# Kernel optimization log

Hardware: AMD Instinct MI355X
Metric: run time of the kernel (lower is better)

The kernel has to match this reference:

```python
import jax, jax.numpy as jnp
import numpy as np

D_MODEL = 2048
N_HEADS = 16
HEAD_DIM = D_MODEL // N_HEADS
SCALE = HEAD_DIM ** -0.5


def setup_inputs() -> dict:
    key = jax.random.key(0)
    ks = jax.random.split(key, 9)
    B, L, D = 4, 4096, D_MODEL
    s = 1.0 / np.sqrt(D)
    inp = {"x": jax.random.normal(ks[0], (B, L, D), dtype=jnp.float32)}
    inp["Wq"] = jax.random.normal(ks[1], (D, D), dtype=jnp.float32) * s
    inp["bq"] = jnp.zeros((D,), dtype=jnp.float32)
    inp["Wk"] = jax.random.normal(ks[2], (D, D), dtype=jnp.float32) * s
    inp["bk"] = jnp.zeros((D,), dtype=jnp.float32)
    inp["Wv"] = jax.random.normal(ks[3], (D, D), dtype=jnp.float32) * s
    inp["bv"] = jnp.zeros((D,), dtype=jnp.float32)
    inp["Wo"] = jax.random.normal(ks[4], (D, D), dtype=jnp.float32) * s
    inp["bo"] = jnp.zeros((D,), dtype=jnp.float32)
    return inp


def reference(x, Wq, bq, Wk, bk, Wv, bv, Wo, bo):
    B, L, D = x.shape
    H, Hd = N_HEADS, HEAD_DIM
    # projections (torch Linear: x @ W.T + b)
    q = jnp.einsum('bld,ed->ble', x, Wq) + bq
    k = jnp.einsum('bld,ed->ble', x, Wk) + bk
    v = jnp.einsum('bld,ed->ble', x, Wv) + bv
    phi_q = jax.nn.elu(q) + 1.0
    phi_k = jax.nn.elu(k) + 1.0
    # (B, L, H, Hd)
    phi_q = phi_q.reshape(B, L, H, Hd)
    phi_k = phi_k.reshape(B, L, H, Hd)
    v = v.reshape(B, L, H, Hd)
    # elementwise prefix sum over sequence dim
    kv_sum = jnp.cumsum(phi_k * v, axis=1)  # (B, L, H, Hd)
    context = (phi_q * kv_sum).reshape(B, L, D) * SCALE
    return jnp.einsum('bld,ed->ble', context, Wo) + bo
```

## Files before the change

kernel.cpp:

```cpp
#include <hip/hip_runtime.h>
#include <hip/hip_bf16.h>
#include <cstdint>
#include <cstddef>

typedef __bf16 bf16x8 __attribute__((ext_vector_type(8)));
typedef __bf16 bf16x4 __attribute__((ext_vector_type(4)));
typedef float  f32x4  __attribute__((ext_vector_type(4)));

#define D_MODEL 2048
#define SEQ     4096
#define BATCH   4
#define M_TOK   (BATCH * SEQ)
#define ATTN_SCALE 0.08838834764831845f

#define BM 128
#define BN 128
#define BK 64

#define NSEG   64
#define SEGLEN (SEQ / NSEG)

__device__ __forceinline__ void async_load16(const void* g, void* l) {
    __builtin_amdgcn_global_load_lds(
        (const __attribute__((address_space(1))) unsigned int*)g,
        (__attribute__((address_space(3))) unsigned int*)l,
        16, 0, 0);
}

__global__ __launch_bounds__(256) void k_cast_bf16(const float* __restrict__ in,
                                                   __bf16* __restrict__ out,
                                                   int n8) {
    int i = blockIdx.x * 256 + threadIdx.x;
    if (i >= n8) return;
    const float4* in4 = (const float4*)in;
    float4 a = in4[2 * i];
    float4 b = in4[2 * i + 1];
    bf16x8 o;
    o[0] = (__bf16)a.x; o[1] = (__bf16)a.y; o[2] = (__bf16)a.z; o[3] = (__bf16)a.w;
    o[4] = (__bf16)b.x; o[5] = (__bf16)b.y; o[6] = (__bf16)b.z; o[7] = (__bf16)b.w;
    ((bf16x8*)out)[i] = o;
}

__global__ __launch_bounds__(256) void k_cast_w4(const float* __restrict__ w0,
                                                 const float* __restrict__ w1,
                                                 const float* __restrict__ w2,
                                                 const float* __restrict__ w3,
                                                 __bf16* __restrict__ out, int n8) {
    const float* srcs[4] = {w0, w1, w2, w3};
    const float* in = srcs[blockIdx.y];
    __bf16* o = out + (size_t)blockIdx.y * (size_t)n8 * 8;
    int i = blockIdx.x * 256 + threadIdx.x;
    if (i >= n8) return;
    const float4* in4 = (const float4*)in;
    float4 a = in4[2 * i];
    float4 b = in4[2 * i + 1];
    bf16x8 v;
    v[0] = (__bf16)a.x; v[1] = (__bf16)a.y; v[2] = (__bf16)a.z; v[3] = (__bf16)a.w;
    v[4] = (__bf16)b.x; v[5] = (__bf16)b.y; v[6] = (__bf16)b.z; v[7] = (__bf16)b.w;
    ((bf16x8*)o)[i] = v;
}

template <int PHI, typename OUT_T>
__device__ __forceinline__ void gemm_bt(const __bf16* __restrict__ A,
                                        const __bf16* __restrict__ Bm,
                                        const float* __restrict__ bias,
                                        OUT_T* __restrict__ C,
                                        int K, int N) {
    __shared__ __align__(16) __bf16 As[BM * BK];
    __shared__ __align__(16) __bf16 Bs[BN * BK];

    const int tid  = threadIdx.x;
    const int lane = tid & 63;
    const int wave = tid >> 6;
    const int waveM = wave & 1;
    const int waveN = wave >> 1;
    const long bm = (long)blockIdx.y * BM;
    const long bn = (long)blockIdx.x * BN;

    const int srow  = tid >> 3;
    const int sphys = tid & 7;
    const __bf16* gA[4]; const __bf16* gB[4];
    __bf16* lA[4]; __bf16* lB[4];
#pragma unroll
    for (int q = 0; q < 4; q++) {
        int r  = q * 32 + srow;
        int cb = (sphys ^ (r & 7)) * 8;
        gA[q] = A  + (bm + r) * (long)K + cb;
        gB[q] = Bm + (bn + r) * (long)K + cb;
        lA[q] = As + q * 2048 + tid * 8;
        lB[q] = Bs + q * 2048 + tid * 8;
    }

    const int mrow = waveM * 64 + (lane & 15);
    const int nrow = waveN * 64 + (lane & 15);
    const int ksel = lane >> 4;

    f32x4 acc[4][4] = {};

    for (int k0 = 0; k0 < K; k0 += BK) {
#pragma unroll
        for (int q = 0; q < 4; q++) async_load16(gA[q] + k0, lA[q]);
#pragma unroll
        for (int q = 0; q < 4; q++) async_load16(gB[q] + k0, lB[q]);
        __syncthreads();

#pragma unroll
        for (int s = 0; s < 2; s++) {
            bf16x8 af[4], bfr[4];
#pragma unroll
            for (int i = 0; i < 4; i++) {
                int r = mrow + i * 16;
                int p = (s * 4 + ksel) ^ (r & 7);
                af[i] = *(const bf16x8*)(As + r * 64 + p * 8);
            }
#pragma unroll
            for (int j = 0; j < 4; j++) {
                int r = nrow + j * 16;
                int p = (s * 4 + ksel) ^ (r & 7);
                bfr[j] = *(const bf16x8*)(Bs + r * 64 + p * 8);
            }
#pragma unroll
            for (int i = 0; i < 4; i++)
#pragma unroll
                for (int j = 0; j < 4; j++)
                    acc[i][j] = __builtin_amdgcn_mfma_f32_16x16x32_bf16(
                        af[i], bfr[j], acc[i][j], 0, 0, 0);
        }
        __syncthreads();
    }

    const int r0 = (lane >> 4) * 4;
    const int cn = lane & 15;
#pragma unroll
    for (int i = 0; i < 4; i++) {
        long mg = bm + waveM * 64 + i * 16 + r0;
#pragma unroll
        for (int j = 0; j < 4; j++) {
            long ng = bn + waveN * 64 + j * 16 + cn;
            float bia = bias[ng];
#pragma unroll
            for (int r = 0; r < 4; r++) {
                float v = acc[i][j][r] + bia;
                if (PHI) v = (v > 0.f) ? (v + 1.f) : __expf(v);
                C[(mg + r) * (long)N + ng] = (OUT_T)v;
            }
        }
    }
}

__global__ __launch_bounds__(256) void k_gemm_qkv(
    const __bf16* __restrict__ xb,
    const __bf16* __restrict__ wq, const __bf16* __restrict__ wk, const __bf16* __restrict__ wv,
    const float* __restrict__ bq, const float* __restrict__ bk, const float* __restrict__ bv,
    __bf16* __restrict__ oq, __bf16* __restrict__ ok, __bf16* __restrict__ ov) {
    const int z = blockIdx.z;
    const __bf16* W = (z == 0) ? wq : (z == 1) ? wk : wv;
    const float*  b = (z == 0) ? bq : (z == 1) ? bk : bv;
    __bf16*       o = (z == 0) ? oq : (z == 1) ? ok : ov;
    if (z < 2)
        gemm_bt<1, __bf16>(xb, W, b, o, D_MODEL, D_MODEL);
    else
        gemm_bt<0, __bf16>(xb, W, b, o, D_MODEL, D_MODEL);
}

__global__ __launch_bounds__(256) void k_gemm_out(
    const __bf16* __restrict__ ctx, const __bf16* __restrict__ wo,
    const float* __restrict__ bo, float* __restrict__ out) {
    gemm_bt<0, float>(ctx, wo, bo, out, D_MODEL, D_MODEL);
}

__global__ __launch_bounds__(256) void k_scan_partial(
    const __bf16* __restrict__ phik, const __bf16* __restrict__ v,
    float* __restrict__ partial) {
    const int b  = blockIdx.z;
    const int s  = blockIdx.y;
    const int c0 = blockIdx.x * 1024 + threadIdx.x * 4;
    long base = ((long)b * SEQ + (long)s * SEGLEN) * D_MODEL + c0;
    const bf16x4* pk = (const bf16x4*)(phik + base);
    const bf16x4* pv = (const bf16x4*)(v + base);
    float s0 = 0, s1 = 0, s2 = 0, s3 = 0;
    for (int l = 0; l < SEGLEN; l++) {
        bf16x4 a = *pk, w = *pv;
        s0 += (float)a[0] * (float)w[0];
        s1 += (float)a[1] * (float)w[1];
        s2 += (float)a[2] * (float)w[2];
        s3 += (float)a[3] * (float)w[3];
        pk += D_MODEL / 4; pv += D_MODEL / 4;
    }
    *(float4*)(partial + ((long)(b * NSEG + s)) * D_MODEL + c0) = make_float4(s0, s1, s2, s3);
}

__global__ __launch_bounds__(256) void k_scan_apply(
    const __bf16* __restrict__ phiq,
    __bf16* phik_ctx,
    const __bf16* __restrict__ v,
    const float* __restrict__ partial) {
    const int b  = blockIdx.z;
    const int s  = blockIdx.y;
    const int c0 = blockIdx.x * 1024 + threadIdx.x * 4;
    float r0 = 0, r1 = 0, r2 = 0, r3 = 0;
    for (int sp = 0; sp < s; sp++) {
        float4 p = *(const float4*)(partial + ((long)(b * NSEG + sp)) * D_MODEL + c0);
        r0 += p.x; r1 += p.y; r2 += p.z; r3 += p.w;
    }
    long base = ((long)b * SEQ + (long)s * SEGLEN) * D_MODEL + c0;
    bf16x4* pk = (bf16x4*)(phik_ctx + base);
    const bf16x4* pv = (const bf16x4*)(v + base);
    const bf16x4* pq = (const bf16x4*)(phiq + base);
    for (int l = 0; l < SEGLEN; l++) {
        bf16x4 a = *pk, w = *pv, q = *pq;
        r0 += (float)a[0] * (float)w[0];
        r1 += (float)a[1] * (float)w[1];
        r2 += (float)a[2] * (float)w[2];
        r3 += (float)a[3] * (float)w[3];
        bf16x4 o;
        o[0] = (__bf16)((float)q[0] * r0 * ATTN_SCALE);
        o[1] = (__bf16)((float)q[1] * r1 * ATTN_SCALE);
        o[2] = (__bf16)((float)q[2] * r2 * ATTN_SCALE);
        o[3] = (__bf16)((float)q[3] * r3 * ATTN_SCALE);
        *pk = o;
        pk += D_MODEL / 4; pv += D_MODEL / 4; pq += D_MODEL / 4;
    }
}

extern "C" void kernel_launch(void* const* d_in, const int* in_sizes, int n_in,
                              void* d_out, int out_size, void* d_ws, size_t ws_size,
                              hipStream_t stream) {
    const float* x  = (const float*)d_in[0];
    const float* Wq = (const float*)d_in[1];
    const float* bq = (const float*)d_in[2];
    const float* Wk = (const float*)d_in[3];
    const float* bk = (const float*)d_in[4];
    const float* Wv = (const float*)d_in[5];
    const float* bv = (const float*)d_in[6];
    const float* Wo = (const float*)d_in[7];
    const float* bo = (const float*)d_in[8];

    const size_t XB = (size_t)M_TOK * D_MODEL;
    const size_t WB = (size_t)D_MODEL * D_MODEL;

    char* p = (char*)d_ws;
    __bf16* xb   = (__bf16*)p; p += XB * 2;
    __bf16* wqb  = (__bf16*)p; p += WB * 2;
    __bf16* wkb  = (__bf16*)p; p += WB * 2;
    __bf16* wvb  = (__bf16*)p; p += WB * 2;
    __bf16* wob  = (__bf16*)p; p += WB * 2;
    __bf16* phiq = (__bf16*)p; p += XB * 2;
    __bf16* phik = (__bf16*)p; p += XB * 2;
    __bf16* vb   = (__bf16*)p; p += XB * 2;
    if ((size_t)(p - (char*)d_ws) > ws_size) return;

    float*  partial = (float*)xb;
    __bf16* ctx     = phik;

    k_cast_bf16<<<dim3((unsigned)(XB / 8 / 256)), 256, 0, stream>>>(x, xb, (int)(XB / 8));
    k_cast_w4<<<dim3((unsigned)(WB / 8 / 256), 4), 256, 0, stream>>>(Wq, Wk, Wv, Wo, wqb, (int)(WB / 8));

    k_gemm_qkv<<<dim3(D_MODEL / BN, M_TOK / BM, 3), 256, 0, stream>>>(
        xb, wqb, wkb, wvb, bq, bk, bv, phiq, phik, vb);

    k_scan_partial<<<dim3(2, NSEG, BATCH), 256, 0, stream>>>(phik, vb, partial);
    k_scan_apply<<<dim3(2, NSEG, BATCH), 256, 0, stream>>>(phiq, phik, vb, partial);

    k_gemm_out<<<dim3(D_MODEL / BN, M_TOK / BM, 1), 256, 0, stream>>>(
        ctx, wob, bo, (float*)d_out);
}
```

Measured before the change: 928.9 us.

## Fuse QKV projections into one 768-thread block sharing the A tile

The QKV GEMM now runs one 768-thread block per output tile, with three wave groups computing Q, K and V from a single shared A tile. This removes the triple loading of x from global memory into LDS. BK is halved to 32 with a new XOR swizzle, and launch bounds request 4 blocks per CU to raise occupancy. The scan segment count is doubled for more parallelism. In exchange, each k-step carries less work per barrier, and the larger block may limit residency.

After: 1.099 ms. 18.4% more time.

```diff
diff --git a/kernel.cpp b/kernel.cpp
--- a/kernel.cpp
+++ b/kernel.cpp
@@ -15,9 +15,9 @@
 
 #define BM 128
 #define BN 128
-#define BK 64
-
-#define NSEG   64
+#define BK 32
+
+#define NSEG   128
 #define SEGLEN (SEQ / NSEG)
 
 __device__ __forceinline__ void async_load16(const void* g, void* l) {
@@ -26,6 +26,7 @@
         (__attribute__((address_space(3))) unsigned int*)l,
         16, 0, 0);
 }
+__device__ __forceinline__ int swz(int r) { return (r >> 1) & 3; }
 
 __global__ __launch_bounds__(256) void k_cast_bf16(const float* __restrict__ in,
                                                    __bf16* __restrict__ out,
@@ -60,12 +61,99 @@
     ((bf16x8*)o)[i] = v;
 }
 
-template <int PHI, typename OUT_T>
-__device__ __forceinline__ void gemm_bt(const __bf16* __restrict__ A,
-                                        const __bf16* __restrict__ Bm,
-                                        const float* __restrict__ bias,
-                                        OUT_T* __restrict__ C,
-                                        int K, int N) {
+__global__ __launch_bounds__(768, 4) void k_gemm_qkv(
+    const __bf16* __restrict__ A,
+    const __bf16* __restrict__ wq, const __bf16* __restrict__ wk, const __bf16* __restrict__ wv,
+    const float* __restrict__ bq, const float* __restrict__ bk, const float* __restrict__ bv,
+    __bf16* __restrict__ oq, __bf16* __restrict__ ok, __bf16* __restrict__ ov) {
+    __shared__ __align__(16) __bf16 As[BM * BK];
+    __shared__ __align__(16) __bf16 Bs[3 * BN * BK];
+
+    const int tid  = threadIdx.x;
+    const int lane = tid & 63;
+    const int wave = tid >> 6;
+    const int zw   = wave >> 2;
+    const int quad = wave & 3;
+    const int waveM = quad & 1;
+    const int waveN = quad >> 1;
+    const long bm = (long)blockIdx.y * BM;
+    const long bn = (long)blockIdx.x * BN;
+    const int K = D_MODEL, N = D_MODEL;
+
+    const int ar = tid >> 2, apc = tid & 3;
+    const __bf16* gA = A + (bm + ar) * (long)K + (long)((apc ^ swz(ar)) * 8);
+    __bf16* lA = As + tid * 8;
+    const __bf16* gB[2]; __bf16* lB[2];
+#pragma unroll
+    for (int u = 0; u < 2; u++) {
+        int cb = tid + u * 768;
+        int z  = cb >> 9;
+        int w  = cb & 511;
+        int r  = w >> 2, pc = w & 3;
+        const __bf16* Wz = (z == 0) ? wq : (z == 1) ? wk : wv;
+        gB[u] = Wz + (bn + r) * (long)K + (long)((pc ^ swz(r)) * 8);
+        lB[u] = Bs + cb * 8;
+    }
+
+    const int ksel = lane >> 4;
+    int offA[4], offB[4];
+#pragma unroll
+    for (int i = 0; i < 4; i++) {
+        int r = waveM * 64 + (lane & 15) + 16 * i;
+        offA[i] = r * BK + (ksel ^ swz(r)) * 8;
+    }
+#pragma unroll
+    for (int j = 0; j < 4; j++) {
+        int r = waveN * 64 + (lane & 15) + 16 * j;
+        offB[j] = zw * (BN * BK) + r * BK + (ksel ^ swz(r)) * 8;
+    }
+
+    f32x4 acc[4][4] = {};
+
+    for (int k0 = 0; k0 < K; k0 += BK) {
+        if (tid < 512) async_load16(gA + k0, lA);
+        async_load16(gB[0] + k0, lB[0]);
+        async_load16(gB[1] + k0, lB[1]);
+        __syncthreads();
+
+        bf16x8 af[4], bfr[4];
+#pragma unroll
+        for (int i = 0; i < 4; i++) af[i]  = *(const bf16x8*)(As + offA[i]);
+#pragma unroll
+        for (int j = 0; j < 4; j++) bfr[j] = *(const bf16x8*)(Bs + offB[j]);
+#pragma unroll
+        for (int i = 0; i < 4; i++)
+#pragma unroll
+            for (int j = 0; j < 4; j++)
+                acc[i][j] = __builtin_amdgcn_mfma_f32_16x16x32_bf16(
+                    af[i], bfr[j], acc[i][j], 0, 0, 0);
+        __syncthreads();
+    }
+
+    const float* bias = (zw == 0) ? bq : (zw == 1) ? bk : bv;
+    __bf16*      Co   = (zw == 0) ? oq : (zw == 1) ? ok : ov;
+    const int r0 = (lane >> 4) * 4;
+    const int cn = lane & 15;
+#pragma unroll
+    for (int i = 0; i < 4; i++) {
+        long mg = bm + waveM * 64 + i * 16 + r0;
+#pragma unroll
+        for (int j = 0; j < 4; j++) {
+            long ng = bn + waveN * 64 + j * 16 + cn;
+            float bia = bias[ng];
+#pragma unroll
+            for (int r = 0; r < 4; r++) {
+                float v = acc[i][j][r] + bia;
+                if (zw < 2) v = (v > 0.f) ? (v + 1.f) : __expf(v);
+                Co[(mg + r) * (long)N + ng] = (__bf16)v;
+            }
+        }
+    }
+}
+
+__global__ __launch_bounds__(256, 4) void k_gemm_out(
+    const __bf16* __restrict__ A, const __bf16* __restrict__ Bm,
+    const float* __restrict__ bias, float* __restrict__ C) {
     __shared__ __align__(16) __bf16 As[BM * BK];
     __shared__ __align__(16) __bf16 Bs[BN * BK];
 
@@ -76,56 +164,53 @@
     const int waveN = wave >> 1;
     const long bm = (long)blockIdx.y * BM;
     const long bn = (long)blockIdx.x * BN;
-
-    const int srow  = tid >> 3;
-    const int sphys = tid & 7;
-    const __bf16* gA[4]; const __bf16* gB[4];
-    __bf16* lA[4]; __bf16* lB[4];
-#pragma unroll
-    for (int q = 0; q < 4; q++) {
-        int r  = q * 32 + srow;
-        int cb = (sphys ^ (r & 7)) * 8;
-        gA[q] = A  + (bm + r) * (long)K + cb;
-        gB[q] = Bm + (bn + r) * (long)K + cb;
-        lA[q] = As + q * 2048 + tid * 8;
-        lB[q] = Bs + q * 2048 + tid * 8;
-    }
-
-    const int mrow = waveM * 64 + (lane & 15);
-    const int nrow = waveN * 64 + (lane & 15);
+    const int K = D_MODEL, N = D_MODEL;
+
+    const __bf16* gA[2]; const __bf16* gB[2]; __bf16* lA[2]; __bf16* lB[2];
+#pragma unroll
+    for (int u = 0; u < 2; u++) {
+        int c = tid + u * 256;
+        int r = c >> 2, pc = c & 3;
+        int co = (pc ^ swz(r)) * 8;
+        gA[u] = A  + (bm + r) * (long)K + co;
+        gB[u] = Bm + (bn + r) * (long)K + co;
+        lA[u] = As + c * 8;
+        lB[u] = Bs + c * 8;
+    }
+
     const int ksel = lane >> 4;
+    int offA[4], offB[4];
+#pragma unroll
+    for (int i = 0; i < 4; i++) {
+        int r = waveM * 64 + (lane & 15) + 16 * i;
+        offA[i] = r * BK + (ksel ^ swz(r)) * 8;
+    }
+#pragma unroll
+    for (int j = 0; j < 4; j++) {
+        int r = waveN * 64 + (lane & 15) + 16 * j;
+        offB[j] = r * BK + (ksel ^ swz(r)) * 8;
+    }
 
     f32x4 acc[4][4] = {};
 
     for (int k0 = 0; k0 < K; k0 += BK) {
 #pragma unroll
-        for (int q = 0; q < 4; q++) async_load16(gA[q] + k0, lA[q]);
-#pragma unroll
-        for (int q = 0; q < 4; q++) async_load16(gB[q] + k0, lB[q]);
+        for (int u = 0; u < 2; u++) { async_load16(gA[u] + k0, lA[u]); }
+#pragma unroll
+        for (int u = 0; u < 2; u++) { async_load16(gB[u] + k0, lB[u]); }
         __syncthreads();
 
-#pragma unroll
-        for (int s = 0; s < 2; s++) {
-            bf16x8 af[4], bfr[4];
-#pragma unroll
-            for (int i = 0; i < 4; i++) {
-                int r = mrow + i * 16;
-                int p = (s * 4 + ksel) ^ (r & 7);
-                af[i] = *(const bf16x8*)(As + r * 64 + p * 8);
-            }
-#pragma unroll
-            for (int j = 0; j < 4; j++) {
-                int r = nrow + j * 16;
-                int p = (s * 4 + ksel) ^ (r & 7);
-                bfr[j] = *(const bf16x8*)(Bs + r * 64 + p * 8);
-            }
-#pragma unroll
-            for (int i = 0; i < 4; i++)
-#pragma unroll
-                for (int j = 0; j < 4; j++)
-                    acc[i][j] = __builtin_amdgcn_mfma_f32_16x16x32_bf16(
-                        af[i], bfr[j], acc[i][j], 0, 0, 0);
-        }
+        bf16x8 af[4], bfr[4];
+#pragma unroll
+        for (int i = 0; i < 4; i++) af[i]  = *(const bf16x8*)(As + offA[i]);
+#pragma unroll
+        for (int j = 0; j < 4; j++) bfr[j] = *(const bf16x8*)(Bs + offB[j]);
+#pragma unroll
+        for (int i = 0; i < 4; i++)
+#pragma unroll
+            for (int j = 0; j < 4; j++)
+                acc[i][j] = __builtin_amdgcn_mfma_f32_16x16x32_bf16(
+                    af[i], bfr[j], acc[i][j], 0, 0, 0);
         __syncthreads();
     }
 
@@ -139,34 +224,10 @@
             long ng = bn + waveN * 64 + j * 16 + cn;
             float bia = bias[ng];
 #pragma unroll
-            for (int r = 0; r < 4; r++) {
-                float v = acc[i][j][r] + bia;
-                if (PHI) v = (v > 0.f) ? (v + 1.f) : __expf(v);
-                C[(mg + r) * (long)N + ng] = (OUT_T)v;
-            }
+            for (int r = 0; r < 4; r++)
+                C[(mg + r) * (long)N + ng] = acc[i][j][r] + bia;
         }
     }
-}
-
-__global__ __launch_bounds__(256) void k_gemm_qkv(
-    const __bf16* __restrict__ xb,
-    const __bf16* __restrict__ wq, const __bf16* __restrict__ wk, const __bf16* __restrict__ wv,
-    const float* __restrict__ bq, const float* __restrict__ bk, const float* __restrict__ bv,
-    __bf16* __restrict__ oq, __bf16* __restrict__ ok, __bf16* __restrict__ ov) {
-    const int z = blockIdx.z;
-    const __bf16* W = (z == 0) ? wq : (z == 1) ? wk : wv;
-    const float*  b = (z == 0) ? bq : (z == 1) ? bk : bv;
-    __bf16*       o = (z == 0) ? oq : (z == 1) ? ok : ov;
-    if (z < 2)
-        gemm_bt<1, __bf16>(xb, W, b, o, D_MODEL, D_MODEL);
-    else
-        gemm_bt<0, __bf16>(xb, W, b, o, D_MODEL, D_MODEL);
-}
-
-__global__ __launch_bounds__(256) void k_gemm_out(
-    const __bf16* __restrict__ ctx, const __bf16* __restrict__ wo,
-    const float* __restrict__ bo, float* __restrict__ out) {
-    gemm_bt<0, float>(ctx, wo, bo, out, D_MODEL, D_MODEL);
 }
 
 __global__ __launch_bounds__(256) void k_scan_partial(
@@ -256,12 +317,12 @@
     k_cast_bf16<<<dim3((unsigned)(XB / 8 / 256)), 256, 0, stream>>>(x, xb, (int)(XB / 8));
     k_cast_w4<<<dim3((unsigned)(WB / 8 / 256), 4), 256, 0, stream>>>(Wq, Wk, Wv, Wo, wqb, (int)(WB / 8));
 
-    k_gemm_qkv<<<dim3(D_MODEL / BN, M_TOK / BM, 3), 256, 0, stream>>>(
+    k_gemm_qkv<<<dim3(D_MODEL / BN, M_TOK / BM), 768, 0, stream>>>(
         xb, wqb, wkb, wvb, bq, bk, bv, phiq, phik, vb);
 
     k_scan_partial<<<dim3(2, NSEG, BATCH), 256, 0, stream>>>(phik, vb, partial);
     k_scan_apply<<<dim3(2, NSEG, BATCH), 256, 0, stream>>>(phiq, phik, vb, partial);
 
-    k_gemm_out<<<dim3(D_MODEL / BN, M_TOK / BM, 1), 256, 0, stream>>>(
+    k_gemm_out<<<dim3(D_MODEL / BN, M_TOK / BM), 256, 0, stream>>>(
         ctx, wob, bo, (float*)d_out);
 }
```
